# Kernel optimization log

Measured on AMD Instinct MI355X. Metric: run time of the kernel, lower is better.

The kernel has to match this reference:

```python
import jax, jax.numpy as jnp
import numpy as np

NUM_EMBEDDINGS = 1024
EMBEDDING_DIM = 256
COMMITMENT_COST = 0.25


def setup_inputs() -> dict:
    key = jax.random.key(0)
    k1, k2 = jax.random.split(key)
    inputs = jax.random.normal(k1, (64, 256, 32, 32), dtype=jnp.float32)
    # nn.Embedding weight init: uniform(-1/K, 1/K)
    embedding = jax.random.uniform(
        k2, (NUM_EMBEDDINGS, EMBEDDING_DIM), dtype=jnp.float32,
        minval=-1.0 / NUM_EMBEDDINGS, maxval=1.0 / NUM_EMBEDDINGS)
    return {"inputs": inputs, "embedding": embedding}


def reference(inputs, embedding):
    # NCHW -> NHWC, flatten to [N, D]
    x = jnp.transpose(inputs, (0, 2, 3, 1))  # [B,H,W,D]
    input_shape = x.shape
    flat = x.reshape(-1, EMBEDDING_DIM)  # [N, D]

    # squared euclidean distances to all codebook entries: [N, K]
    distances = (jnp.sum(flat ** 2, axis=1, keepdims=True)
                 + jnp.sum(embedding ** 2, axis=1)
                 - 2.0 * flat @ embedding.T)
    idx = jnp.argmin(distances, axis=1)  # [N]

    # one-hot encodings (returned output); quantization via gather is
    # mathematically identical to encodings @ embedding
    encodings = jax.nn.one_hot(idx, NUM_EMBEDDINGS, dtype=embedding.dtype)  # [N,K]
    quantized_flat = embedding[idx]  # [N, D]
    quantized = quantized_flat.reshape(input_shape)  # [B,H,W,D]

    e_latent_loss = jnp.mean((jax.lax.stop_gradient(quantized) - x) ** 2)
    q_latent_loss = jnp.mean((quantized - jax.lax.stop_gradient(x)) ** 2)
    loss = q_latent_loss + COMMITMENT_COST * e_latent_loss

    # straight-through estimator
    quantized_st = x + jax.lax.stop_gradient(quantized - x)

    avg_probs = jnp.mean(encodings, axis=0)  # [K]
    perplexity = jnp.exp(-jnp.sum(avg_probs * jnp.log(avg_probs + 1e-10)))

    quantized_out = jnp.transpose(quantized_st, (0, 3, 1, 2))  # NHWC -> NCHW
    return (loss, quantized_out, perplexity, encodings, quantized_flat)
```

## Files before the change

### kernel.cpp

```cpp
#include <hip/hip_runtime.h>
#include <hip/hip_bf16.h>
#include <math.h>

#define NB    64
#define D     256
#define K     1024
#define HW    1024
#define NTOT  65536
#define MARGIN 1e-5f

#define OUT_QOUT   1
#define OUT_PERP   16777217
#define OUT_ENC    16777218
#define OUT_QFLAT  83886082


typedef __attribute__((ext_vector_type(8))) short bf16x8;
typedef __attribute__((ext_vector_type(4))) float f32x4;

__global__ void enorm_kernel(const float* __restrict__ emb, float* __restrict__ enorm) {
    int k = blockIdx.x * 256 + threadIdx.x;
    const float4* row = (const float4*)(emb + (size_t)k * D);
    float s = 0.f;
    #pragma unroll
    for (int q = 0; q < D / 4; q++) {
        float4 v = row[q];
        s += v.x * v.x + v.y * v.y + v.z * v.z + v.w * v.w;
    }
    enorm[k] = s;
}

__global__ void esplit_kernel(const float* __restrict__ emb, ushort* __restrict__ efrag) {
    const int ntg = blockIdx.x;
    const int t = threadIdx.x;
    __shared__ float sEm[16 * 260];

    {
        const int row = t >> 4, seg = t & 15;
        const float4* src = (const float4*)(emb + (size_t)(ntg * 16 + row) * D + seg * 16);
        float4* dst = (float4*)(sEm + row * 260 + seg * 16);
        #pragma unroll
        for (int q = 0; q < 4; q++) dst[q] = src[q];
    }
    __syncthreads();

    const int w = t >> 6, lane = t & 63;
    for (int fb = w; fb < 16; fb += 4) {
        const int h = fb >> 3, dc = fb & 7;
        const float* srcp = sEm + (lane & 15) * 260 + dc * 32 + (lane >> 4) * 8;
        ushort o[8];
        #pragma unroll
        for (int j = 0; j < 8; j++) {
            float x = srcp[j];
            __hip_bfloat16 hb = __float2bfloat16(x);
            if (h == 0) { o[j] = *(ushort*)&hb; }
            else {
                float hf = __bfloat162float(hb);
                __hip_bfloat16 lb = __float2bfloat16(x - hf);
                o[j] = *(ushort*)&lb;
            }
        }
        ushort* dst = efrag + ((size_t)(h * 64 + ntg) * 8 + dc) * 512 + lane * 8;
        *(int4*)dst = *(int4*)o;
    }
}

__global__ __launch_bounds__(256, 4) void score_mfma_kernel(
    const float* __restrict__ in, const ushort* __restrict__ efrag,
    const float* __restrict__ enorm, int* __restrict__ idx,
    int* __restrict__ rcount, int* __restrict__ rlist)
{
    __shared__ ushort sA[16384];

    const int t = threadIdx.x;
    const int n0 = blockIdx.x * 32;
    const int b = n0 >> 10, p0 = n0 & 1023;

    {
        const float* src = in + (size_t)b * (D * HW) + (size_t)t * HW + p0;
        const int quad = (t >> 3) & 3, dc = t >> 5, j = t & 7;
        #pragma unroll
        for (int g = 0; g < 2; g++) {
            float xs[16];
            #pragma unroll
            for (int q = 0; q < 4; q++) {
                float4 v = ((const float4*)src)[g * 4 + q];
                xs[q * 4 + 0] = v.x; xs[q * 4 + 1] = v.y; xs[q * 4 + 2] = v.z; xs[q * 4 + 3] = v.w;
            }
            #pragma unroll
            for (int mm = 0; mm < 16; mm++) {
                float x = xs[mm];
                __hip_bfloat16 hb = __float2bfloat16(x);
                float hf = __bfloat162float(hb);
                __hip_bfloat16 lb = __float2bfloat16(x - hf);
                const int l = mm + 16 * quad;
                sA[((0 * 2 + g) * 8 + dc) * 512 + l * 8 + j] = *(ushort*)&hb;
                sA[((1 * 2 + g) * 8 + dc) * 512 + l * 8 + j] = *(ushort*)&lb;
            }
        }
    }
    __syncthreads();

    const int w = t >> 6, lane = t & 63;

    float rm1 = 3.4e38f, rm2 = 3.4e38f; int ri = 0;

    for (int kp = 0; kp < 4; kp++) {
        f32x4 acc[2][4];
        #pragma unroll
        for (int mt = 0; mt < 2; mt++)
            #pragma unroll
            for (int ntl = 0; ntl < 4; ntl++) acc[mt][ntl] = (f32x4){0.f, 0.f, 0.f, 0.f};

        bf16x8 bh[4], nbh[4];
        #pragma unroll
        for (int ntl = 0; ntl < 4; ntl++) {
            const int ntg = kp * 16 + w * 4 + ntl;
            bh[ntl] = *(const bf16x8*)(efrag + ((size_t)ntg * 8 + 0) * 512 + lane * 8);
        }
        for (int dc = 0; dc < 8; dc++) {
            bf16x8 bl[4];
            #pragma unroll
            for (int ntl = 0; ntl < 4; ntl++) {
                const int ntg = kp * 16 + w * 4 + ntl;
                const size_t off = ((size_t)ntg * 8 + dc) * 512 + lane * 8;
                bl[ntl] = *(const bf16x8*)(efrag + off + 262144);
                if (dc < 7) nbh[ntl] = *(const bf16x8*)(efrag + off + 512);
            }
            #pragma unroll
            for (int mt = 0; mt < 2; mt++) {
                bf16x8 ah = *(const bf16x8*)(sA + ((0 * 2 + mt) * 8 + dc) * 512 + lane * 8);
                bf16x8 al = *(const bf16x8*)(sA + ((1 * 2 + mt) * 8 + dc) * 512 + lane * 8);
                #pragma unroll
                for (int ntl = 0; ntl < 4; ntl++) {
                    acc[mt][ntl] = __builtin_amdgcn_mfma_f32_16x16x32_bf16(al, bh[ntl], acc[mt][ntl], 0, 0, 0);
                    acc[mt][ntl] = __builtin_amdgcn_mfma_f32_16x16x32_bf16(ah, bh[ntl], acc[mt][ntl], 0, 0, 0);
                    acc[mt][ntl] = __builtin_amdgcn_mfma_f32_16x16x32_bf16(ah, bl[ntl], acc[mt][ntl], 0, 0, 0);
                }
            }
            if (dc < 7) {
                #pragma unroll
                for (int ntl = 0; ntl < 4; ntl++) bh[ntl] = nbh[ntl];
            }
        }

        float env[4]; int kc[4];
        #pragma unroll
        for (int ntl = 0; ntl < 4; ntl++) {
            kc[ntl] = kp * 256 + (w * 4 + ntl) * 16 + (lane & 15);
            env[ntl] = enorm[kc[ntl]];
        }
        #pragma unroll
        for (int mt = 0; mt < 2; mt++)
            #pragma unroll
            for (int r = 0; r < 4; r++) {
                float m1 = 3.4e38f, m2 = 3.4e38f; int i1 = 0;
                #pragma unroll
                for (int ntl = 0; ntl < 4; ntl++) {
                    float s = env[ntl] - 2.0f * acc[mt][ntl][r];
                    if (s < m1) { m2 = m1; m1 = s; i1 = kc[ntl]; }
                    else if (s < m2) m2 = s;
                }
                #pragma unroll
                for (int mask = 1; mask <= 8; mask <<= 1) {
                    float o1 = __shfl_xor(m1, mask, 64);
                    int   oi = __shfl_xor(i1, mask, 64);
                    float o2 = __shfl_xor(m2, mask, 64);
                    float n2 = fminf(fminf(m2, o2), fmaxf(m1, o1));
                    if (o1 < m1 || (o1 == m1 && oi < i1)) { m1 = o1; i1 = oi; }
                    m2 = n2;
                }
                if ((lane & 15) == mt * 4 + r) {
                    float n2 = fminf(fminf(rm2, m2), fmaxf(rm1, m1));
                    if (m1 < rm1 || (m1 == rm1 && i1 < ri)) { rm1 = m1; ri = i1; }
                    rm2 = n2;
                }
            }
    }

    __syncthreads();
    float* sM1 = (float*)sA;
    float* sM2 = sM1 + 128;
    int*   sI  = (int*)(sM2 + 128);
    if ((lane & 15) < 8) {
        const int row = ((lane & 15) >> 2) * 16 + (lane >> 4) * 4 + (lane & 3);
        sM1[w * 32 + row] = rm1;
        sM2[w * 32 + row] = rm2;
        sI [w * 32 + row] = ri;
    }
    __syncthreads();
    if (t < 32) {
        float b1 = sM1[t], b2 = sM2[t]; int bi = sI[t];
        #pragma unroll
        for (int ww = 1; ww < 4; ww++) {
            float a1 = sM1[ww * 32 + t], a2 = sM2[ww * 32 + t]; int ai = sI[ww * 32 + t];
            float n2 = fminf(fminf(b2, a2), fmaxf(b1, a1));
            if (a1 < b1 || (a1 == b1 && ai < bi)) { b1 = a1; bi = ai; }
            b2 = n2;
        }
        const int n = n0 + t;
        idx[n] = bi;
        if (b2 - b1 < MARGIN) {
            int pos = atomicAdd(rcount, 1);
            rlist[pos] = n;
        }
    }
}

__global__ void rescue_kernel(const float* __restrict__ in, const float* __restrict__ emb,
                              const int* __restrict__ rcount, const int* __restrict__ rlist,
                              int* __restrict__ idx)
{
    const int wid = blockIdx.x * 4 + (threadIdx.x >> 6);
    const int lane = threadIdx.x & 63;
    const int count = *rcount;
    for (int li = wid; li < count; li += 512 * 4) {
        const int n = rlist[li];
        const int b = n >> 10, p = n & 1023;
        const float* f = in + (size_t)b * (D * HW) + p;
        float fr[4];
        #pragma unroll
        for (int q = 0; q < 4; q++) fr[q] = f[(size_t)(lane + q * 64) * HW];
        double bm = 1e300; int bk = 0;
        #pragma unroll 1
        for (int kk = 0; kk < 16; kk++) {
            const int k = lane + kk * 64;
            const float4* er4 = (const float4*)(emb + (size_t)k * D);
            double sc[4];
            #pragma unroll
            for (int q = 0; q < 4; q++) sc[q] = 0.0;
            #pragma unroll
            for (int q = 0; q < 4; q++) {
                #pragma unroll
                for (int f4 = 0; f4 < 16; f4++) {
                    const float4 ev4 = er4[q * 16 + f4];
                    #pragma unroll
                    for (int e = 0; e < 4; e++) {
                        const int dl = f4 * 4 + e;
                        const double fv = (double)__shfl(fr[q], dl, 64);
                        const double ev = (double)((const float*)&ev4)[e];
                        sc[q] += ev * (ev - 2.0 * fv);
                    }
                }
            }
            const double s = (sc[0] + sc[1]) + (sc[2] + sc[3]);
            if (s < bm) { bm = s; bk = k; }
        }
        #pragma unroll
        for (int off = 32; off >= 1; off >>= 1) {
            double om = __shfl_xor(bm, off, 64);
            int    ok = __shfl_xor(bk, off, 64);
            if (om < bm || (om == bm && ok < bk)) { bm = om; bk = ok; }
        }
        if (lane == 0) idx[n] = bk;
    }
}

__global__ __launch_bounds__(256) void outputs_kernel(
    const float* __restrict__ in, const float* __restrict__ emb,
    const int* __restrict__ idx, float* __restrict__ out,
    double* __restrict__ lossPartial, int* __restrict__ hist)
{
    __shared__ int skv[32];
    __shared__ float sQ[32 * 260];
    __shared__ double sred[4];

    const int t = threadIdx.x;
    const int n0 = blockIdx.x * 32;
    const int b = n0 >> 10, p0 = n0 & 1023;

    if (t < 32) skv[t] = idx[n0 + t];
    __syncthreads();

    {
        const int r = t >> 3, c0 = (t & 7) * 32;
        const int kv = skv[r];
        const float4* src = (const float4*)(emb + (size_t)kv * D + c0);
        float4* dstL = (float4*)(sQ + r * 260 + c0);
        float4* dstG = (float4*)(out + OUT_QFLAT + (size_t)(n0 + r) * D + c0);
        #pragma unroll
        for (int g = 0; g < 8; g++) {
            float4 v = src[g];
            dstL[g] = v;
            dstG[g] = v;
        }
    }
    {
        float* encBase = out + OUT_ENC + (size_t)n0 * K;
        const int c0 = t * 4;
        #pragma unroll 4
        for (int r = 0; r < 32; r++) {
            const int kv = skv[r];
            float4 v = make_float4(0.f, 0.f, 0.f, 0.f);
            if (kv >= c0 && kv < c0 + 4) ((float*)&v)[kv - c0] = 1.0f;
            *(float4*)(encBase + (size_t)r * K + c0) = v;
        }
    }
    if (t < 32) atomicAdd(&hist[skv[t]], 1);
    __syncthreads();

    const int p = t & 31, dg = t >> 5;
    double acc = 0.0;
    const size_t obase = (size_t)b * (D * HW) + p0 + p;
    #pragma unroll
    for (int dd = 0; dd < 32; dd++) {
        const int d = dg * 32 + dd;
        const float q = sQ[p * 260 + d];
        const float x = in[obase + (size_t)d * HW];
        out[OUT_QOUT + obase + (size_t)d * HW] = q;
        const float df = q - x;
        acc += (double)(df * df);
    }
    #pragma unroll
    for (int off = 32; off >= 1; off >>= 1) acc += __shfl_xor(acc, off, 64);
    if ((t & 63) == 0) sred[t >> 6] = acc;
    __syncthreads();
    if (t == 0) lossPartial[blockIdx.x] = sred[0] + sred[1] + sred[2] + sred[3];
}

__global__ void finalize_kernel(const int* __restrict__ hist, const double* __restrict__ lossPartial,
                                float* __restrict__ out)
{
    const int t = threadIdx.x;
    double s = 0.0;
    #pragma unroll
    for (int q = 0; q < 4; q++) {
        const int c = hist[t + q * 256];
        const double p = (double)c / (double)NTOT;
        s += p * log(p + 1e-10);
    }
    double l = 0.0;
    #pragma unroll
    for (int q = 0; q < 8; q++) l += lossPartial[t + q * 256];
    #pragma unroll
    for (int off = 32; off >= 1; off >>= 1) {
        s += __shfl_xor(s, off, 64);
        l += __shfl_xor(l, off, 64);
    }
    __shared__ double sr[4], lr[4];
    if ((t & 63) == 0) { sr[t >> 6] = s; lr[t >> 6] = l; }
    __syncthreads();
    if (t == 0) {
        out[0] = (float)(1.25 * (lr[0] + lr[1] + lr[2] + lr[3]) / (double)(NTOT * (size_t)D));
        out[OUT_PERP] = (float)exp(-(sr[0] + sr[1] + sr[2] + sr[3]));
    }
}

extern "C" void kernel_launch(void* const* d_in, const int* in_sizes, int n_in,
                              void* d_out, int out_size, void* d_ws, size_t ws_size,
                              hipStream_t stream)
{
    const float* in  = (const float*)d_in[0];
    const float* emb = (const float*)d_in[1];
    float* out = (float*)d_out;
    char* ws = (char*)d_ws;

    int*    rcount      = (int*)(ws + 0);
    int*    hist        = (int*)(ws + 16);
    float*  enorm       = (float*)(ws + 4112);
    int*    idx         = (int*)(ws + 8208);
    int*    rlist       = (int*)(ws + 270352);
    double* lossPartial = (double*)(ws + 532496);
    ushort* efrag       = (ushort*)(ws + 548880);

    hipMemsetAsync(ws, 0, 8208, stream);

    enorm_kernel<<<K / 256, 256, 0, stream>>>(emb, enorm);
    esplit_kernel<<<K / 16, 256, 0, stream>>>(emb, efrag);
    score_mfma_kernel<<<NTOT / 32, 256, 0, stream>>>(in, efrag, enorm, idx, rcount, rlist);
    rescue_kernel<<<512, 256, 0, stream>>>(in, emb, rcount, rlist, idx);
    outputs_kernel<<<NTOT / 32, 256, 0, stream>>>(in, emb, idx, out, lossPartial, hist);
    finalize_kernel<<<1, 256, 0, stream>>>(hist, lossPartial, out);
}
```

Measured before the change: 1.010 ms.

## Restructure A-tile staging and software-pipeline codebook fragment loads across MFMA loop

The A staging now has each thread gather 8 strided floats and write whole 16-byte fragments to shared memory, replacing scattered 2-byte stores. The MFMA loop is fully unrolled and split into two half-tiles of two column tiles each. Both the hi and lo bf16 codebook fragments for the next half-tile, including across kp boundaries, are prefetched while the current half computes. This is meant to hide global-load latency and cut LDS store overhead, but it uses uncoalesced strided global reads in the staging phase and adds register pressure.

Measured after the change: 1.039 ms. 1.03x slower.

```diff
diff --git a/kernel.cpp b/kernel.cpp
--- a/kernel.cpp
+++ b/kernel.cpp
@@ -75,80 +75,92 @@
     const int t = threadIdx.x;
     const int n0 = blockIdx.x * 32;
     const int b = n0 >> 10, p0 = n0 & 1023;
-
-    {
-        const float* src = in + (size_t)b * (D * HW) + (size_t)t * HW + p0;
-        const int quad = (t >> 3) & 3, dc = t >> 5, j = t & 7;
-        #pragma unroll
-        for (int g = 0; g < 2; g++) {
-            float xs[16];
-            #pragma unroll
-            for (int q = 0; q < 4; q++) {
-                float4 v = ((const float4*)src)[g * 4 + q];
-                xs[q * 4 + 0] = v.x; xs[q * 4 + 1] = v.y; xs[q * 4 + 2] = v.z; xs[q * 4 + 3] = v.w;
-            }
-            #pragma unroll
-            for (int mm = 0; mm < 16; mm++) {
-                float x = xs[mm];
+    const int w = t >> 6, lane = t & 63;
+
+    {
+        #pragma unroll
+        for (int i = 0; i < 4; i++) {
+            const int fb = w * 4 + i;
+            const int mt = fb >> 3, dc = fb & 7;
+            const int m  = mt * 16 + (lane & 15);
+            const int d0 = dc * 32 + (lane >> 4) * 8;
+            const float* src = in + (size_t)b * (D * HW) + (size_t)d0 * HW + p0 + m;
+            ushort oh[8], ol[8];
+            #pragma unroll
+            for (int j = 0; j < 8; j++) {
+                const float x = src[(size_t)j * HW];
                 __hip_bfloat16 hb = __float2bfloat16(x);
-                float hf = __bfloat162float(hb);
+                const float hf = __bfloat162float(hb);
                 __hip_bfloat16 lb = __float2bfloat16(x - hf);
-                const int l = mm + 16 * quad;
-                sA[((0 * 2 + g) * 8 + dc) * 512 + l * 8 + j] = *(ushort*)&hb;
-                sA[((1 * 2 + g) * 8 + dc) * 512 + l * 8 + j] = *(ushort*)&lb;
-            }
-        }
-    }
-    __syncthreads();
-
-    const int w = t >> 6, lane = t & 63;
+                oh[j] = *(ushort*)&hb;
+                ol[j] = *(ushort*)&lb;
+            }
+            ushort* dh = sA + ((0 * 2 + mt) * 8 + dc) * 512 + lane * 8;
+            ushort* dl = sA + ((1 * 2 + mt) * 8 + dc) * 512 + lane * 8;
+            *(int4*)dh = *(int4*)oh;
+            *(int4*)dl = *(int4*)ol;
+        }
+    }
+    __syncthreads();
 
     float rm1 = 3.4e38f, rm2 = 3.4e38f; int ri = 0;
+
+    const ushort* efragLo = efrag + 262144;
+
+    bf16x8 bh[2], bl[2], nbh[2], nbl[2];
+    {
+        const size_t o0 = ((size_t)((0 * 16 + w * 4 + 0) * 8 + 0)) * 512 + lane * 8;
+        const size_t o1 = ((size_t)((0 * 16 + w * 4 + 1) * 8 + 0)) * 512 + lane * 8;
+        bh[0] = *(const bf16x8*)(efrag + o0);  bl[0] = *(const bf16x8*)(efragLo + o0);
+        bh[1] = *(const bf16x8*)(efrag + o1);  bl[1] = *(const bf16x8*)(efragLo + o1);
+    }
 
     for (int kp = 0; kp < 4; kp++) {
         f32x4 acc[2][4];
         #pragma unroll
         for (int mt = 0; mt < 2; mt++)
             #pragma unroll
-            for (int ntl = 0; ntl < 4; ntl++) acc[mt][ntl] = (f32x4){0.f, 0.f, 0.f, 0.f};
-
-        bf16x8 bh[4], nbh[4];
-        #pragma unroll
-        for (int ntl = 0; ntl < 4; ntl++) {
-            const int ntg = kp * 16 + w * 4 + ntl;
-            bh[ntl] = *(const bf16x8*)(efrag + ((size_t)ntg * 8 + 0) * 512 + lane * 8);
-        }
+            for (int c = 0; c < 4; c++) acc[mt][c] = (f32x4){0.f, 0.f, 0.f, 0.f};
+
+        #pragma unroll
         for (int dc = 0; dc < 8; dc++) {
-            bf16x8 bl[4];
-            #pragma unroll
-            for (int ntl = 0; ntl < 4; ntl++) {
-                const int ntg = kp * 16 + w * 4 + ntl;
-                const size_t off = ((size_t)ntg * 8 + dc) * 512 + lane * 8;
-                bl[ntl] = *(const bf16x8*)(efrag + off + 262144);
-                if (dc < 7) nbh[ntl] = *(const bf16x8*)(efrag + off + 512);
-            }
+            bf16x8 ah[2], al[2];
             #pragma unroll
             for (int mt = 0; mt < 2; mt++) {
-                bf16x8 ah = *(const bf16x8*)(sA + ((0 * 2 + mt) * 8 + dc) * 512 + lane * 8);
-                bf16x8 al = *(const bf16x8*)(sA + ((1 * 2 + mt) * 8 + dc) * 512 + lane * 8);
+                ah[mt] = *(const bf16x8*)(sA + ((0 * 2 + mt) * 8 + dc) * 512 + lane * 8);
+                al[mt] = *(const bf16x8*)(sA + ((1 * 2 + mt) * 8 + dc) * 512 + lane * 8);
+            }
+            #pragma unroll
+            for (int nh = 0; nh < 2; nh++) {
+                {
+                    int nkp = kp, ndc = dc, nnh = nh + 1;
+                    if (nnh == 2) { nnh = 0; ndc = dc + 1; if (ndc == 8) { ndc = 0; nkp = (kp + 1) & 3; } }
+                    const int ntg0 = nkp * 16 + w * 4 + nnh * 2;
+                    const size_t o0 = ((size_t)(ntg0 * 8 + ndc)) * 512 + lane * 8;
+                    const size_t o1 = o0 + 8 * 512;
+                    nbh[0] = *(const bf16x8*)(efrag + o0);  nbl[0] = *(const bf16x8*)(efragLo + o0);
+                    nbh[1] = *(const bf16x8*)(efrag + o1);  nbl[1] = *(const bf16x8*)(efragLo + o1);
+                }
                 #pragma unroll
-                for (int ntl = 0; ntl < 4; ntl++) {
-                    acc[mt][ntl] = __builtin_amdgcn_mfma_f32_16x16x32_bf16(al, bh[ntl], acc[mt][ntl], 0, 0, 0);
-                    acc[mt][ntl] = __builtin_amdgcn_mfma_f32_16x16x32_bf16(ah, bh[ntl], acc[mt][ntl], 0, 0, 0);
-                    acc[mt][ntl] = __builtin_amdgcn_mfma_f32_16x16x32_bf16(ah, bl[ntl], acc[mt][ntl], 0, 0, 0);
-                }
-            }
-            if (dc < 7) {
-                #pragma unroll
-                for (int ntl = 0; ntl < 4; ntl++) bh[ntl] = nbh[ntl];
+                for (int mt = 0; mt < 2; mt++) {
+                    #pragma unroll
+                    for (int ntl = 0; ntl < 2; ntl++) {
+                        const int c = nh * 2 + ntl;
+                        acc[mt][c] = __builtin_amdgcn_mfma_f32_16x16x32_bf16(al[mt], bh[ntl], acc[mt][c], 0, 0, 0);
+                        acc[mt][c] = __builtin_amdgcn_mfma_f32_16x16x32_bf16(ah[mt], bh[ntl], acc[mt][c], 0, 0, 0);
+                        acc[mt][c] = __builtin_amdgcn_mfma_f32_16x16x32_bf16(ah[mt], bl[ntl], acc[mt][c], 0, 0, 0);
+                    }
+                }
+                bh[0] = nbh[0]; bl[0] = nbl[0];
+                bh[1] = nbh[1]; bl[1] = nbl[1];
             }
         }
 
         float env[4]; int kc[4];
         #pragma unroll
-        for (int ntl = 0; ntl < 4; ntl++) {
-            kc[ntl] = kp * 256 + (w * 4 + ntl) * 16 + (lane & 15);
-            env[ntl] = enorm[kc[ntl]];
+        for (int c = 0; c < 4; c++) {
+            kc[c] = kp * 256 + (w * 4 + c) * 16 + (lane & 15);
+            env[c] = enorm[kc[c]];
         }
         #pragma unroll
         for (int mt = 0; mt < 2; mt++)
@@ -156,9 +168,9 @@
             for (int r = 0; r < 4; r++) {
                 float m1 = 3.4e38f, m2 = 3.4e38f; int i1 = 0;
                 #pragma unroll
-                for (int ntl = 0; ntl < 4; ntl++) {
-                    float s = env[ntl] - 2.0f * acc[mt][ntl][r];
-                    if (s < m1) { m2 = m1; m1 = s; i1 = kc[ntl]; }
+                for (int c = 0; c < 4; c++) {
+                    float s = env[c] - 2.0f * acc[mt][c][r];
+                    if (s < m1) { m2 = m1; m1 = s; i1 = kc[c]; }
                     else if (s < m2) m2 = s;
                 }
                 #pragma unroll
```
